# Performance work log

Measured on AMD Instinct MI355X. Metric: run time of the kernel, lower is better.

Reference implementation:

```python
import jax, jax.numpy as jnp
import numpy as np

N, H, I, B = 128, 128, 2, 8192

def _gru(x, h, Wih, Whh, bih, bhh):
    # torch.nn.GRUCell semantics; gates ordered (r, z, n)
    gi = x @ Wih.T + bih              # [B, 3H]
    gh = h @ Whh.T + bhh              # [B, 3H]
    ir, iz, ic = jnp.split(gi, 3, axis=1)
    hr, hz, hc = jnp.split(gh, 3, axis=1)
    r = jax.nn.sigmoid(ir + hr)
    z = jax.nn.sigmoid(iz + hz)
    n = jnp.tanh(ic + r * hc)
    return (1.0 - z) * n + z * h

def setup_inputs() -> dict:
    key = jax.random.key(0)
    ks = jax.random.split(key, 13)
    s = 0.1  # ~1/sqrt(H) init scale
    return {
        "inputs": jax.random.uniform(ks[0], (B, I), jnp.float32),
        "Wih0": jax.random.normal(ks[1], (N, 3 * H, I), jnp.float32) * s,
        "Whh0": jax.random.normal(ks[2], (N, 3 * H, H), jnp.float32) * s,
        "bih0": jax.random.normal(ks[3], (N, 3 * H), jnp.float32) * s,
        "bhh0": jax.random.normal(ks[4], (N, 3 * H), jnp.float32) * s,
        "Wih1": jax.random.normal(ks[5], (N, 3 * H, H), jnp.float32) * s,
        "Whh1": jax.random.normal(ks[6], (N, 3 * H, H), jnp.float32) * s,
        "bih1": jax.random.normal(ks[7], (N, 3 * H), jnp.float32) * s,
        "bhh1": jax.random.normal(ks[8], (N, 3 * H), jnp.float32) * s,
        "W1": jax.random.normal(ks[9], (N, H, H), jnp.float32) * s,
        "b1": jax.random.normal(ks[10], (N, H), jnp.float32) * s,
        "W2": jax.random.normal(ks[11], (N, I, H), jnp.float32) * s,
        "b2": jax.random.normal(ks[12], (N, I), jnp.float32) * s,
    }

def reference(inputs, Wih0, Whh0, bih0, bhh0, Wih1, Whh1, bih1, bhh1, W1, b1, W2, b2):
    batch = inputs.shape[0]
    h0 = jnp.zeros((batch, H), inputs.dtype)
    sample_keys = jax.random.split(jax.random.key(42), N)

    def step(carry, xs):
        inp, h1, h2 = carry
        (wih0, whh0, bi0, bh0, wih1, whh1, bi1, bh1, w1, bb1, w2, bb2, k) = xs
        h1 = _gru(inp, h1, wih0, whh0, bi0, bh0)
        h2 = _gru(h1, h2, wih1, whh1, bi1, bh1)
        s = jnp.cos(h2) + 1e-10
        hdn = jax.nn.relu(s @ w1.T + bb1)
        p = jax.nn.softmax(hdn @ w2.T + bb2, axis=1) + 1e-10  # probs + eps, as in torch
        sample = jax.lax.stop_gradient(jax.random.categorical(k, jnp.log(p)))
        nxt = jax.nn.one_hot(sample, I, dtype=p.dtype)
        return (nxt, h1, h2), p

    xs = (Wih0, Whh0, bih0, bhh0, Wih1, Whh1, bih1, bhh1, W1, b1, W2, b2, sample_keys)
    _, probs = jax.lax.scan(step, (inputs, h0, h0), xs)  # probs: [N, B, I]
    return jnp.transpose(probs, (1, 0, 2))  # [B, N, I]
```

## Files before the change

### kernel.cpp

```cpp
#include <hip/hip_runtime.h>
#include <cstdint>


namespace {

constexpr int NSTEPS = 128;
constexpr int HDIM = 128;
constexpr int G3H = 384;

constexpr int BTM = 32;
constexpr int THM = 512;
constexpr int S0P = 385;
constexpr int S1P = 513;

constexpr int BT = 16;
constexpr int THREADS = 256;
constexpr int HP = 132;
constexpr int SP = 516;

typedef _Float16 half8 __attribute__((ext_vector_type(8)));
typedef float f32x4 __attribute__((ext_vector_type(4)));

constexpr float LO_SCALE = 4096.0f;
constexpr float LO_INV = 2.44140625e-4f;
constexpr float F16_MIN_NORM = 6.104e-5f;
constexpr float LOG2E = 1.4426950408889634f;
constexpr float INV2PI = 0.15915494309189535f;

__device__ __forceinline__ void split_f16(float x, _Float16& a1, _Float16& a2s) {
  _Float16 h = (fabsf(x) < F16_MIN_NORM) ? (_Float16)0.0f : (_Float16)x;
  a1 = h;
  a2s = (_Float16)((x - (float)h) * LO_SCALE);
}

__device__ __forceinline__ void tf2x32(uint32_t k0, uint32_t k1,
                                       uint32_t x0, uint32_t x1,
                                       uint32_t& o0, uint32_t& o1) {
  const uint32_t ks2 = k0 ^ k1 ^ 0x1BD11BDAu;
  uint32_t v0 = x0 + k0;
  uint32_t v1 = x1 + k1;
  const uint32_t ks[3] = {k0, k1, ks2};
  const uint32_t rotA[4] = {13u, 15u, 26u, 6u};
  const uint32_t rotB[4] = {17u, 29u, 16u, 24u};
#pragma unroll
  for (int i = 0; i < 5; ++i) {
#pragma unroll
    for (int j = 0; j < 4; ++j) {
      const uint32_t r = (i & 1) ? rotB[j] : rotA[j];
      v0 += v1;
      v1 = (v1 << r) | (v1 >> (32u - r));
      v1 ^= v0;
    }
    v0 += ks[(i + 1) % 3];
    v1 += ks[(i + 2) % 3] + (uint32_t)(i + 1);
  }
  o0 = v0;
  o1 = v1;
}

__device__ __forceinline__ float u01_from_bits(uint32_t bits) {
  const float tiny = 1.1754943508222875e-38f;
  float f = __uint_as_float((bits >> 9) | 0x3F800000u) - 1.0f;
  float u = f * (1.0f - tiny) + tiny;
  return fmaxf(tiny, u);
}

__device__ __forceinline__ float fexp2(float x) { return __builtin_amdgcn_exp2f(x); }
__device__ __forceinline__ float frcp(float x) { return __builtin_amdgcn_rcpf(x); }
__device__ __forceinline__ float sigmoidf(float x) {
  return frcp(1.0f + fexp2(-LOG2E * x));
}
__device__ __forceinline__ float ftanhf(float x) {
  return 1.0f - 2.0f * frcp(1.0f + fexp2((2.0f * LOG2E) * x));
}
__device__ __forceinline__ float fcosx(float x) {
  return __builtin_amdgcn_cosf(x * INV2PI);
}

__device__ __forceinline__ float dot4(const float4 a, const float4 b, float c) {
  c = fmaf(a.x, b.x, c);
  c = fmaf(a.y, b.y, c);
  c = fmaf(a.z, b.z, c);
  c = fmaf(a.w, b.w, c);
  return c;
}

__device__ __forceinline__ void load_Afrag(const _Float16* arr, int lane,
                                           half8 (&A)[2][4]) {
#pragma unroll
  for (int mt = 0; mt < 2; ++mt)
#pragma unroll
    for (int kt = 0; kt < 4; ++kt)
      A[mt][kt] = *(const half8*)(arr + mt * 2048 + (kt * 64 + lane) * 8);
}

__device__ __forceinline__ void load_B(const _Float16* __restrict__ B1,
                                       const _Float16* __restrict__ B2,
                                       int jt, int lane,
                                       half8 (&b1)[4], half8 (&b2)[4]) {
#pragma unroll
  for (int kt = 0; kt < 4; ++kt) {
    const size_t o = ((size_t)(jt * 4 + kt) * 64 + lane) * 8;
    b1[kt] = *(const half8*)(B1 + o);
    b2[kt] = *(const half8*)(B2 + o);
  }
}

__device__ __forceinline__ void mfma_regs(const half8 (&A1)[2][4],
                                          const half8 (&A2)[2][4],
                                          const half8 (&b1)[4],
                                          const half8 (&b2)[4],
                                          f32x4 (&c1)[2], f32x4 (&c2)[2]) {
#pragma unroll
  for (int kt = 0; kt < 4; ++kt)
#pragma unroll
    for (int mt = 0; mt < 2; ++mt) {
      c1[mt] = __builtin_amdgcn_mfma_f32_16x16x32_f16(A1[mt][kt], b1[kt], c1[mt], 0, 0, 0);
      c2[mt] = __builtin_amdgcn_mfma_f32_16x16x32_f16(A1[mt][kt], b2[kt], c2[mt], 0, 0, 0);
      c2[mt] = __builtin_amdgcn_mfma_f32_16x16x32_f16(A2[mt][kt], b1[kt], c2[mt], 0, 0, 0);
    }
}

}

extern "C" __global__ __launch_bounds__(256)
void preprocess_split_kernel(const float* __restrict__ src,
                             _Float16* __restrict__ d1,
                             _Float16* __restrict__ d2,
                             int total, int JT) {
  const int idx = blockIdx.x * 256 + threadIdx.x;
  if (idx >= total) return;
  const int lane = idx & 63;
  const int kt = (idx >> 6) & 3;
  const int rest = idx >> 8;
  const int jt = rest % JT;
  const int nstep = rest / JT;

  const int j = jt * 16 + (lane & 15);
  const int k0 = kt * 32 + ((lane >> 4) << 3);
  const float* p = src + ((size_t)nstep * (JT * 16) + j) * 128 + k0;
  const float4 w0 = *(const float4*)p;
  const float4 w1 = *(const float4*)(p + 4);
  const float xs[8] = {w0.x, w0.y, w0.z, w0.w, w1.x, w1.y, w1.z, w1.w};

  half8 o1, o2;
#pragma unroll
  for (int t = 0; t < 8; ++t) {
    _Float16 a1, a2s;
    split_f16(xs[t], a1, a2s);
    o1[t] = a1;
    o2[t] = a2s;
  }
  *(half8*)(d1 + (size_t)idx * 8) = o1;
  *(half8*)(d2 + (size_t)idx * 8) = o2;
}

extern "C" __global__ __launch_bounds__(512, 2)
void rnn_wavefn_mfma_kernel(const float* __restrict__ inputs,
                            const float* __restrict__ Wih0,
                            const float* __restrict__ bih0,
                            const float* __restrict__ bhh0,
                            const float* __restrict__ bih1,
                            const float* __restrict__ bhh1,
                            const float* __restrict__ b1,
                            const float* __restrict__ W2,
                            const float* __restrict__ b2,
                            const _Float16* __restrict__ Whh0_1,
                            const _Float16* __restrict__ Whh0_2,
                            const _Float16* __restrict__ Wih1_1,
                            const _Float16* __restrict__ Wih1_2,
                            const _Float16* __restrict__ Whh1_1,
                            const _Float16* __restrict__ Whh1_2,
                            const _Float16* __restrict__ W1_1,
                            const _Float16* __restrict__ W1_2,
                            float* __restrict__ out) {
  __shared__ __align__(16) float S0[BTM][S0P];
  __shared__ float S1[BTM][S1P];
  __shared__ _Float16 h1A1[4096], h1A2[4096];
  __shared__ _Float16 h2A1[4096], h2A2[4096];
  __shared__ float xin[BTM][2];
  __shared__ uint32_t skey[NSTEPS][2];

  _Float16* const csA1 = (_Float16*)&S0[0][0];
  _Float16* const csA2 = csA1 + 4096;

  const int tid = threadIdx.x;
  const int b0 = blockIdx.x * BTM;
  const int wv = tid >> 6;
  const int lane = tid & 63;
  const int lm = lane & 15;
  const int m0 = (lane >> 4) * 4;

  const int cb = tid & 31;
  const int ct5 = tid >> 5;
  const int d0 = ct5 * 8;
  const int ibase = ((cb >> 4) * 2048 +
                     (((ct5 >> 2) << 6) + ((ct5 & 3) << 4) + (cb & 15)) * 8);

  float h1r[8], h2r[8];
#pragma unroll
  for (int i = 0; i < 8; ++i) { h1r[i] = 0.0f; h2r[i] = 0.0f; }
  for (int i = tid; i < 4096; i += THM) {
    h1A1[i] = (_Float16)0.0f; h1A2[i] = (_Float16)0.0f;
    h2A1[i] = (_Float16)0.0f; h2A2[i] = (_Float16)0.0f;
  }
  if (tid < BTM * 2) {
    xin[tid >> 1][tid & 1] = inputs[(b0 + (tid >> 1)) * 2 + (tid & 1)];
  }
  if (tid < NSTEPS) {
    uint32_t a, bk;
    tf2x32(0u, 42u, 0u, (uint32_t)tid, a, bk);
    skey[tid][0] = a;
    skey[tid][1] = bk;
  }
  __syncthreads();

  auto do_out = [&](int np) {
    const float* __restrict__ W2p = W2 + (size_t)np * 2 * HDIM;
    const float* __restrict__ b2p = b2 + (size_t)np * 2;
    const int ln = tid & 15;
    const int ob = tid >> 4;
    const int kb = ln * 8;
    float a0 = 0.0f, a1 = 0.0f;
#pragma unroll
    for (int k = 0; k < 8; ++k) {
      const float hd = S1[ob][384 + kb + k];
      a0 = fmaf(W2p[kb + k], hd, a0);
      a1 = fmaf(W2p[HDIM + kb + k], hd, a1);
    }
#pragma unroll
    for (int off = 8; off >= 1; off >>= 1) {
      a0 += __shfl_xor(a0, off, 16);
      a1 += __shfl_xor(a1, off, 16);
    }
    if (ln < 2) {
      const float l0 = a0 + b2p[0];
      const float l1 = a1 + b2p[1];
      const float m = fmaxf(l0, l1);
      const float e0 = expf(l0 - m);
      const float e1 = expf(l1 - m);
      const float sum = e0 + e1;
      const float p0 = e0 / sum + 1e-10f;
      const float p1 = e1 / sum + 1e-10f;
      const int gb = b0 + ob;
      uint32_t o0, o1;
      tf2x32(skey[np][0], skey[np][1], 0u, (uint32_t)(2 * gb + ln), o0, o1);
      const float u = u01_from_bits(o0 ^ o1);
      const float g = -logf(-logf(u));
      const float zv = logf((ln == 0) ? p0 : p1) + g;
      const float zo = __shfl_xor(zv, 1, 16);
      if (ln == 0) {
        out[((size_t)gb * NSTEPS + np) * 2 + 0] = p0;
        out[((size_t)gb * NSTEPS + np) * 2 + 1] = p1;
        const int smp = (zo > zv) ? 1 : 0;
        xin[ob][0] = (smp == 0) ? 1.0f : 0.0f;
        xin[ob][1] = (smp == 1) ? 1.0f : 0.0f;
      }
    }
  };

  half8 Bb1[2][4], Bb2[2][4];
  load_B(Whh0_1, Whh0_2, wv * 3, lane, Bb1[0], Bb2[0]);

  for (int n = 0; n < NSTEPS; ++n) {
    const float* __restrict__ Wih0n = Wih0 + (size_t)n * G3H * 2;
    const float* __restrict__ bih0n = bih0 + (size_t)n * G3H;
    const float* __restrict__ bhh0n = bhh0 + (size_t)n * G3H;
    const float* __restrict__ bih1n = bih1 + (size_t)n * G3H;
    const float* __restrict__ bhh1n = bhh1 + (size_t)n * G3H;
    const float* __restrict__ b1n = b1 + (size_t)n * HDIM;
    const size_t fo3 = (size_t)n * 49152;
    const size_t fo1 = (size_t)n * 16384;

    {
      half8 A1[2][4], A2[2][4];
      load_Afrag(h1A1, lane, A1);
      load_Afrag(h1A2, lane, A2);
      float bv[6];
#pragma unroll
      for (int t = 0; t < 6; ++t)
        bv[t] = ((t < 3) ? bhh0n : bhh1n)[(wv * 3 + (t % 3)) * 16 + lm];
#pragma unroll
      for (int t = 0; t < 6; ++t) {
        const int cur = t & 1;
        if (t < 5) {
          const int tn = t + 1;
          const _Float16* nB1 = (tn < 3) ? (Whh0_1 + fo3) : (Whh1_1 + fo3);
          const _Float16* nB2 = (tn < 3) ? (Whh0_2 + fo3) : (Whh1_2 + fo3);
          load_B(nB1, nB2, wv * 3 + (tn % 3), lane, Bb1[cur ^ 1], Bb2[cur ^ 1]);
        }
        if (t == 3) {
          load_Afrag(h2A1, lane, A1);
          load_Afrag(h2A2, lane, A2);
        }
        const int jt = wv * 3 + (t % 3);
        f32x4 c1[2] = {{0.f,0.f,0.f,0.f},{0.f,0.f,0.f,0.f}};
        f32x4 c2[2] = {{0.f,0.f,0.f,0.f},{0.f,0.f,0.f,0.f}};
        mfma_regs(A1, A2, Bb1[cur], Bb2[cur], c1, c2);
        const int col = jt * 16 + lm;
        if (t < 3) {
#pragma unroll
          for (int mt = 0; mt < 2; ++mt)
#pragma unroll
            for (int r = 0; r < 4; ++r)
              S0[mt * 16 + m0 + r][col] = bv[t] + fmaf(c2[mt][r], LO_INV, c1[mt][r]);
        } else {
#pragma unroll
          for (int mt = 0; mt < 2; ++mt)
#pragma unroll
            for (int r = 0; r < 4; ++r)
              S1[mt * 16 + m0 + r][col] = bv[t] + fmaf(c2[mt][r], LO_INV, c1[mt][r]);
        }
      }
    }
    if (n > 0) do_out(n - 1);
    __syncthreads();

    {
      load_B(Wih1_1 + fo3, Wih1_2 + fo3, wv * 3, lane, Bb1[0], Bb2[0]);
      const float x0 = xin[cb][0];
      const float x1 = xin[cb][1];
      float wr[16], wz[16], wn[16], br[8], bz[8], bn[8];
#pragma unroll
      for (int q = 0; q < 4; ++q) {
        *(float4*)&wr[q * 4] = *(const float4*)(Wih0n + d0 * 2 + q * 4);
        *(float4*)&wz[q * 4] = *(const float4*)(Wih0n + (d0 + 128) * 2 + q * 4);
        *(float4*)&wn[q * 4] = *(const float4*)(Wih0n + (d0 + 256) * 2 + q * 4);
      }
      *(float4*)&br[0] = *(const float4*)(bih0n + d0);
      *(float4*)&br[4] = *(const float4*)(bih0n + d0 + 4);
      *(float4*)&bz[0] = *(const float4*)(bih0n + 128 + d0);
      *(float4*)&bz[4] = *(const float4*)(bih0n + 128 + d0 + 4);
      *(float4*)&bn[0] = *(const float4*)(bih0n + 256 + d0);
      *(float4*)&bn[4] = *(const float4*)(bih0n + 256 + d0 + 4);
      half8 o1, o2;
#pragma unroll
      for (int j = 0; j < 8; ++j) {
        const int d = d0 + j;
        const float gir = fmaf(wr[2 * j], x0, fmaf(wr[2 * j + 1], x1, br[j]));
        const float giz = fmaf(wz[2 * j], x0, fmaf(wz[2 * j + 1], x1, bz[j]));
        const float gin = fmaf(wn[2 * j], x0, fmaf(wn[2 * j + 1], x1, bn[j]));
        const float r = sigmoidf(gir + S0[cb][d]);
        const float z = sigmoidf(giz + S0[cb][d + 128]);
        const float nn = ftanhf(gin + r * S0[cb][d + 256]);
        const float h1n = (1.0f - z) * nn + z * h1r[j];
        h1r[j] = h1n;
        _Float16 a1, a2s;
        split_f16(h1n, a1, a2s);
        o1[j] = a1;
        o2[j] = a2s;
      }
      *(half8*)(h1A1 + ibase) = o1;
      *(half8*)(h1A2 + ibase) = o2;
    }
    __syncthreads();

    {
      half8 A1[2][4], A2[2][4];
      load_Afrag(h1A1, lane, A1);
      load_Afrag(h1A2, lane, A2);
      float bv[3];
#pragma unroll
      for (int t = 0; t < 3; ++t) bv[t] = bih1n[(wv * 3 + t) * 16 + lm];
#pragma unroll
      for (int t = 0; t < 3; ++t) {
        const int cur = t & 1;
        if (t < 2)
          load_B(Wih1_1 + fo3, Wih1_2 + fo3, wv * 3 + t + 1, lane,
                 Bb1[cur ^ 1], Bb2[cur ^ 1]);
        const int jt = wv * 3 + t;
        f32x4 c1[2] = {{0.f,0.f,0.f,0.f},{0.f,0.f,0.f,0.f}};
        f32x4 c2[2] = {{0.f,0.f,0.f,0.f},{0.f,0.f,0.f,0.f}};
        mfma_regs(A1, A2, Bb1[cur], Bb2[cur], c1, c2);
        const int col = jt * 16 + lm;
        if (jt < 16) {
#pragma unroll
          for (int mt = 0; mt < 2; ++mt)
#pragma unroll
            for (int r = 0; r < 4; ++r)
              S1[mt * 16 + m0 + r][col] += bv[t] + fmaf(c2[mt][r], LO_INV, c1[mt][r]);
        } else {
#pragma unroll
          for (int mt = 0; mt < 2; ++mt)
#pragma unroll
            for (int r = 0; r < 4; ++r)
              S1[mt * 16 + m0 + r][col + 128] = bv[t] + fmaf(c2[mt][r], LO_INV, c1[mt][r]);
        }
      }
    }
    __syncthreads();

    half8 hb1[4], hb2[4];
    {
      load_B(W1_1 + fo1, W1_2 + fo1, wv, lane, hb1, hb2);
      const size_t fo3n = (size_t)((n + 1 < NSTEPS) ? n + 1 : n) * 49152;
      load_B(Whh0_1 + fo3n, Whh0_2 + fo3n, wv * 3, lane, Bb1[0], Bb2[0]);
      half8 o1, o2, p1, p2;
#pragma unroll
      for (int j = 0; j < 8; ++j) {
        const int d = d0 + j;
        const float r = sigmoidf(S1[cb][d]);
        const float z = sigmoidf(S1[cb][d + 128]);
        const float nn = ftanhf(S1[cb][d + 384] + r * S1[cb][d + 256]);
        const float h2n = (1.0f - z) * nn + z * h2r[j];
        h2r[j] = h2n;
        _Float16 a1, a2s;
        split_f16(h2n, a1, a2s);
        o1[j] = a1;
        o2[j] = a2s;
        const float cv = fcosx(h2n) + 1e-10f;
        split_f16(cv, a1, a2s);
        p1[j] = a1;
        p2[j] = a2s;
      }
      *(half8*)(h2A1 + ibase) = o1;
      *(half8*)(h2A2 + ibase) = o2;
      *(half8*)(csA1 + ibase) = p1;
      *(half8*)(csA2 + ibase) = p2;
    }
    __syncthreads();

    {
      const float bias = b1n[wv * 16 + lm];
      half8 A1[2][4], A2[2][4];
      load_Afrag(csA1, lane, A1);
      load_Afrag(csA2, lane, A2);
      f32x4 c1[2] = {{0.f,0.f,0.f,0.f},{0.f,0.f,0.f,0.f}};
      f32x4 c2[2] = {{0.f,0.f,0.f,0.f},{0.f,0.f,0.f,0.f}};
      mfma_regs(A1, A2, hb1, hb2, c1, c2);
      const int col = wv * 16 + lm;
#pragma unroll
      for (int mt = 0; mt < 2; ++mt)
#pragma unroll
        for (int r = 0; r < 4; ++r)
          S1[mt * 16 + m0 + r][384 + col] =
              fmaxf(bias + fmaf(c2[mt][r], LO_INV, c1[mt][r]), 0.0f);
    }
    __syncthreads();
  }

  do_out(NSTEPS - 1);
}

extern "C" __global__ __launch_bounds__(256, 2)
void rnn_wavefn_fp32_kernel(const float* __restrict__ inputs,
                            const float* __restrict__ Wih0,
                            const float* __restrict__ Whh0,
                            const float* __restrict__ bih0,
                            const float* __restrict__ bhh0,
                            const float* __restrict__ Wih1,
                            const float* __restrict__ Whh1,
                            const float* __restrict__ bih1,
                            const float* __restrict__ bhh1,
                            const float* __restrict__ W1,
                            const float* __restrict__ b1,
                            const float* __restrict__ W2,
                            const float* __restrict__ b2,
                            float* __restrict__ out) {
  __shared__ float h1[BT][HP];
  __shared__ float h2[BT][HP];
  __shared__ float S[BT][SP];
  __shared__ float xin[BT][2];

  const int tid = threadIdx.x;
  const int b0 = blockIdx.x * BT;
  const int tj = tid >> 2;
  const int tq = tid & 3;

  for (int i = tid; i < BT * HP; i += THREADS) {
    ((float*)h1)[i] = 0.0f;
    ((float*)h2)[i] = 0.0f;
  }
  if (tid < BT * 2) {
    xin[tid >> 1][tid & 1] = inputs[(b0 + (tid >> 1)) * 2 + (tid & 1)];
  }
  __syncthreads();

  for (int n = 0; n < NSTEPS; ++n) {
    const float* __restrict__ Wih0n = Wih0 + (size_t)n * G3H * 2;
    const float* __restrict__ Whh0n = Whh0 + (size_t)n * G3H * HDIM;
    const float* __restrict__ bih0n = bih0 + (size_t)n * G3H;
    const float* __restrict__ bhh0n = bhh0 + (size_t)n * G3H;
    const float* __restrict__ Wih1n = Wih1 + (size_t)n * G3H * HDIM;
    const float* __restrict__ Whh1n = Whh1 + (size_t)n * G3H * HDIM;
    const float* __restrict__ bih1n = bih1 + (size_t)n * G3H;
    const float* __restrict__ bhh1n = bhh1 + (size_t)n * G3H;
    const float* __restrict__ W1n = W1 + (size_t)n * HDIM * HDIM;
    const float* __restrict__ b1n = b1 + (size_t)n * HDIM;
    const float* __restrict__ W2n = W2 + (size_t)n * 2 * HDIM;
    const float* __restrict__ b2n = b2 + (size_t)n * 2;

    {
      float acc[6][4];
#pragma unroll
      for (int g = 0; g < 6; ++g) {
        const float bias = bhh0n[tj + g * 64];
#pragma unroll
        for (int i = 0; i < 4; ++i) acc[g][i] = bias;
      }
      for (int kk = 0; kk < HDIM; kk += 16) {
#pragma unroll
        for (int s = 0; s < 4; ++s) {
          const int k = kk + s * 4;
          float4 w[6];
#pragma unroll
          for (int g = 0; g < 6; ++g)
            w[g] = *(const float4*)(Whh0n + (size_t)(tj + g * 64) * HDIM + k);
#pragma unroll
          for (int i = 0; i < 4; ++i) {
            const float4 hv = *(const float4*)&h1[tq + 4 * i][k];
#pragma unroll
            for (int g = 0; g < 6; ++g) acc[g][i] = dot4(w[g], hv, acc[g][i]);
          }
        }
      }
#pragma unroll
      for (int g = 0; g < 6; ++g)
#pragma unroll
        for (int i = 0; i < 4; ++i) S[tq + 4 * i][tj + g * 64] = acc[g][i];
    }
    __syncthreads();

#pragma unroll
    for (int rep = 0; rep < (BT * HDIM) / THREADS; ++rep) {
      const int idx = tid + rep * THREADS;
      const int b = idx >> 7;
      const int d = idx & 127;
      const float x0 = xin[b][0];
      const float x1 = xin[b][1];
      const float gir = fmaf(Wih0n[d * 2 + 0], x0, fmaf(Wih0n[d * 2 + 1], x1, bih0n[d]));
      const float giz = fmaf(Wih0n[(d + 128) * 2 + 0], x0,
                             fmaf(Wih0n[(d + 128) * 2 + 1], x1, bih0n[d + 128]));
      const float gin = fmaf(Wih0n[(d + 256) * 2 + 0], x0,
                             fmaf(Wih0n[(d + 256) * 2 + 1], x1, bih0n[d + 256]));
      const float r = sigmoidf(gir + S[b][d]);
      const float z = sigmoidf(giz + S[b][d + 128]);
      const float nn = tanhf(gin + r * S[b][d + 256]);
      h1[b][d] = (1.0f - z) * nn + z * h1[b][d];
    }
    __syncthreads();

    {
      float acc[6][4];
#pragma unroll
      for (int g = 0; g < 6; ++g) {
        const float bias = bhh1n[tj + g * 64];
#pragma unroll
        for (int i = 0; i < 4; ++i) acc[g][i] = bias;
      }
      for (int kk = 0; kk < HDIM; kk += 16) {
#pragma unroll
        for (int s = 0; s < 4; ++s) {
          const int k = kk + s * 4;
          float4 w[6];
#pragma unroll
          for (int g = 0; g < 6; ++g)
            w[g] = *(const float4*)(Whh1n + (size_t)(tj + g * 64) * HDIM + k);
#pragma unroll
          for (int i = 0; i < 4; ++i) {
            const float4 hv = *(const float4*)&h2[tq + 4 * i][k];
#pragma unroll
            for (int g = 0; g < 6; ++g) acc[g][i] = dot4(w[g], hv, acc[g][i]);
          }
        }
      }
#pragma unroll
      for (int g = 0; g < 6; ++g)
#pragma unroll
        for (int i = 0; i < 4; ++i) S[tq + 4 * i][tj + g * 64] = acc[g][i];
    }

    {
      float acc[6][4];
#pragma unroll
      for (int g = 0; g < 6; ++g) {
        const float bias = bih1n[tj + g * 64];
#pragma unroll
        for (int i = 0; i < 4; ++i) acc[g][i] = bias;
      }
      for (int kk = 0; kk < HDIM; kk += 16) {
#pragma unroll
        for (int s = 0; s < 4; ++s) {
          const int k = kk + s * 4;
          float4 w[6];
#pragma unroll
          for (int g = 0; g < 6; ++g)
            w[g] = *(const float4*)(Wih1n + (size_t)(tj + g * 64) * HDIM + k);
#pragma unroll
          for (int i = 0; i < 4; ++i) {
            const float4 hv = *(const float4*)&h1[tq + 4 * i][k];
#pragma unroll
            for (int g = 0; g < 6; ++g) acc[g][i] = dot4(w[g], hv, acc[g][i]);
          }
        }
      }
#pragma unroll
      for (int g = 0; g < 6; ++g) {
        const int row = tj + g * 64;
#pragma unroll
        for (int i = 0; i < 4; ++i) {
          if (row < 256) S[tq + 4 * i][row] += acc[g][i];
          else           S[tq + 4 * i][row + 128] = acc[g][i];
        }
      }
    }
    __syncthreads();

#pragma unroll
    for (int rep = 0; rep < (BT * HDIM) / THREADS; ++rep) {
      const int idx = tid + rep * THREADS;
      const int b = idx >> 7;
      const int d = idx & 127;
      const float r = sigmoidf(S[b][d]);
      const float z = sigmoidf(S[b][d + 128]);
      const float nn = tanhf(S[b][d + 384] + r * S[b][d + 256]);
      const float h2n = (1.0f - z) * nn + z * h2[b][d];
      h2[b][d] = h2n;
      S[b][d] = cosf(h2n) + 1e-10f;
    }
    __syncthreads();

    {
      float acc[2][4];
#pragma unroll
      for (int g = 0; g < 2; ++g) {
        const float bias = b1n[tj + g * 64];
#pragma unroll
        for (int i = 0; i < 4; ++i) acc[g][i] = bias;
      }
      for (int kk = 0; kk < HDIM; kk += 16) {
#pragma unroll
        for (int s = 0; s < 4; ++s) {
          const int k = kk + s * 4;
          float4 w[2];
          w[0] = *(const float4*)(W1n + (size_t)(tj)*HDIM + k);
          w[1] = *(const float4*)(W1n + (size_t)(tj + 64) * HDIM + k);
#pragma unroll
          for (int i = 0; i < 4; ++i) {
            const float4 sv = *(const float4*)&S[tq + 4 * i][k];
            acc[0][i] = dot4(w[0], sv, acc[0][i]);
            acc[1][i] = dot4(w[1], sv, acc[1][i]);
          }
        }
      }
#pragma unroll
      for (int g = 0; g < 2; ++g)
#pragma unroll
        for (int i = 0; i < 4; ++i)
          S[tq + 4 * i][384 + tj + g * 64] = fmaxf(acc[g][i], 0.0f);
    }
    __syncthreads();

    {
      const int ln = tid & 15;
      const int b = tid >> 4;
      const int kb = ln * 8;
      float a0 = 0.0f, a1 = 0.0f;
#pragma unroll
      for (int k = 0; k < 8; ++k) {
        const float hd = S[b][384 + kb + k];
        a0 = fmaf(W2n[kb + k], hd, a0);
        a1 = fmaf(W2n[HDIM + kb + k], hd, a1);
      }
#pragma unroll
      for (int off = 8; off >= 1; off >>= 1) {
        a0 += __shfl_xor(a0, off, 16);
        a1 += __shfl_xor(a1, off, 16);
      }
      if (ln == 0) {
        const float l0 = a0 + b2n[0];
        const float l1 = a1 + b2n[1];
        const float m = fmaxf(l0, l1);
        const float e0 = expf(l0 - m);
        const float e1 = expf(l1 - m);
        const float sum = e0 + e1;
        const float p0 = e0 / sum + 1e-10f;
        const float p1 = e1 / sum + 1e-10f;
        const int gb = b0 + b;
        out[((size_t)gb * NSTEPS + n) * 2 + 0] = p0;
        out[((size_t)gb * NSTEPS + n) * 2 + 1] = p1;

        uint32_t k0n, k1n;
        tf2x32(0u, 42u, 0u, (uint32_t)n, k0n, k1n);
        uint32_t o0, o1;
        tf2x32(k0n, k1n, 0u, (uint32_t)(2 * gb), o0, o1);
        const float u0 = u01_from_bits(o0 ^ o1);
        tf2x32(k0n, k1n, 0u, (uint32_t)(2 * gb + 1), o0, o1);
        const float u1 = u01_from_bits(o0 ^ o1);
        const float g0 = -logf(-logf(u0));
        const float g1 = -logf(-logf(u1));
        const float z0 = logf(p0) + g0;
        const float z1 = logf(p1) + g1;
        const int smp = (z1 > z0) ? 1 : 0;
        xin[b][0] = (smp == 0) ? 1.0f : 0.0f;
        xin[b][1] = (smp == 1) ? 1.0f : 0.0f;
      }
    }
    __syncthreads();
  }
}

extern "C" void kernel_launch(void* const* d_in, const int* in_sizes, int n_in,
                              void* d_out, int out_size, void* d_ws, size_t ws_size,
                              hipStream_t stream) {
  (void)in_sizes; (void)n_in; (void)out_size;
  const float* inputs = (const float*)d_in[0];
  const float* Wih0 = (const float*)d_in[1];
  const float* Whh0 = (const float*)d_in[2];
  const float* bih0 = (const float*)d_in[3];
  const float* bhh0 = (const float*)d_in[4];
  const float* Wih1 = (const float*)d_in[5];
  const float* Whh1 = (const float*)d_in[6];
  const float* bih1 = (const float*)d_in[7];
  const float* bhh1 = (const float*)d_in[8];
  const float* W1 = (const float*)d_in[9];
  const float* b1 = (const float*)d_in[10];
  const float* W2 = (const float*)d_in[11];
  const float* b2 = (const float*)d_in[12];
  float* out = (float*)d_out;

  constexpr size_t EB = 6291456;
  constexpr size_t EW1 = 2097152;
  constexpr size_t WS_NEEDED = (6 * EB + 2 * EW1) * sizeof(_Float16);

  if (ws_size >= WS_NEEDED) {
    _Float16* w = (_Float16*)d_ws;
    _Float16* Whh0_1 = w;
    _Float16* Whh0_2 = w + EB;
    _Float16* Wih1_1 = w + 2 * EB;
    _Float16* Wih1_2 = w + 3 * EB;
    _Float16* Whh1_1 = w + 4 * EB;
    _Float16* Whh1_2 = w + 5 * EB;
    _Float16* W1_1 = w + 6 * EB;
    _Float16* W1_2 = w + 6 * EB + EW1;

    hipLaunchKernelGGL(preprocess_split_kernel, dim3(3072), dim3(256), 0, stream,
                       Whh0, Whh0_1, Whh0_2, 786432, 24);
    hipLaunchKernelGGL(preprocess_split_kernel, dim3(3072), dim3(256), 0, stream,
                       Wih1, Wih1_1, Wih1_2, 786432, 24);
    hipLaunchKernelGGL(preprocess_split_kernel, dim3(3072), dim3(256), 0, stream,
                       Whh1, Whh1_1, Whh1_2, 786432, 24);
    hipLaunchKernelGGL(preprocess_split_kernel, dim3(1024), dim3(256), 0, stream,
                       W1, W1_1, W1_2, 262144, 8);
    hipLaunchKernelGGL(rnn_wavefn_mfma_kernel, dim3(8192 / BTM), dim3(THM), 0, stream,
                       inputs, Wih0, bih0, bhh0, bih1, bhh1, b1, W2, b2,
                       Whh0_1, Whh0_2, Wih1_1, Wih1_2, Whh1_1, Whh1_2, W1_1, W1_2,
                       out);
  } else {
    hipLaunchKernelGGL(rnn_wavefn_fp32_kernel, dim3(8192 / BT), dim3(THREADS), 0, stream,
                       inputs, Wih0, Whh0, bih0, bhh0, Wih1, Whh1, bih1, bhh1,
                       W1, b1, W2, b2, out);
  }
}
```

Measured before the change: 1.577 ms.

## Double block to 1024 threads and split GRU gate tiles across 16 waves

```diff
diff --git a/kernel.cpp b/kernel.cpp
--- a/kernel.cpp
+++ b/kernel.cpp
@@ -9,7 +9,7 @@
 constexpr int G3H = 384;
 
 constexpr int BTM = 32;
-constexpr int THM = 512;
+constexpr int THM = 1024;
 constexpr int S0P = 385;
 constexpr int S1P = 513;
 
@@ -19,6 +19,7 @@
 constexpr int SP = 516;
 
 typedef _Float16 half8 __attribute__((ext_vector_type(8)));
+typedef _Float16 half4 __attribute__((ext_vector_type(4)));
 typedef float f32x4 __attribute__((ext_vector_type(4)));
 
 constexpr float LO_SCALE = 4096.0f;
@@ -155,7 +156,7 @@
   *(half8*)(d2 + (size_t)idx * 8) = o2;
 }
 
-extern "C" __global__ __launch_bounds__(512, 2)
+extern "C" __global__ __launch_bounds__(1024, 4)
 void rnn_wavefn_mfma_kernel(const float* __restrict__ inputs,
                             const float* __restrict__ Wih0,
                             const float* __restrict__ bih0,
@@ -193,13 +194,14 @@
 
   const int cb = tid & 31;
   const int ct5 = tid >> 5;
-  const int d0 = ct5 * 8;
-  const int ibase = ((cb >> 4) * 2048 +
-                     (((ct5 >> 2) << 6) + ((ct5 & 3) << 4) + (cb & 15)) * 8);
-
-  float h1r[8], h2r[8];
-#pragma unroll
-  for (int i = 0; i < 8; ++i) { h1r[i] = 0.0f; h2r[i] = 0.0f; }
+  const int d0 = ct5 * 4;
+  const int ibase4 = (cb >> 4) * 2048 +
+                     (((ct5 >> 3) << 6) + (((ct5 >> 1) & 3) << 4) + (cb & 15)) * 8 +
+                     (ct5 & 1) * 4;
+
+  float h1r[4], h2r[4];
+#pragma unroll
+  for (int i = 0; i < 4; ++i) { h1r[i] = 0.0f; h2r[i] = 0.0f; }
   for (int i = tid; i < 4096; i += THM) {
     h1A1[i] = (_Float16)0.0f; h1A2[i] = (_Float16)0.0f;
     h2A1[i] = (_Float16)0.0f; h2A2[i] = (_Float16)0.0f;
@@ -218,20 +220,20 @@
   auto do_out = [&](int np) {
     const float* __restrict__ W2p = W2 + (size_t)np * 2 * HDIM;
     const float* __restrict__ b2p = b2 + (size_t)np * 2;
-    const int ln = tid & 15;
-    const int ob = tid >> 4;
-    const int kb = ln * 8;
+    const int ln = tid & 31;
+    const int ob = tid >> 5;
+    const int kb = ln * 4;
     float a0 = 0.0f, a1 = 0.0f;
 #pragma unroll
-    for (int k = 0; k < 8; ++k) {
+    for (int k = 0; k < 4; ++k) {
       const float hd = S1[ob][384 + kb + k];
       a0 = fmaf(W2p[kb + k], hd, a0);
       a1 = fmaf(W2p[HDIM + kb + k], hd, a1);
     }
 #pragma unroll
-    for (int off = 8; off >= 1; off >>= 1) {
-      a0 += __shfl_xor(a0, off, 16);
-      a1 += __shfl_xor(a1, off, 16);
+    for (int off = 16; off >= 1; off >>= 1) {
+      a0 += __shfl_xor(a0, off, 32);
+      a1 += __shfl_xor(a1, off, 32);
     }
     if (ln < 2) {
       const float l0 = a0 + b2p[0];
@@ -248,7 +250,7 @@
       const float u = u01_from_bits(o0 ^ o1);
       const float g = -logf(-logf(u));
       const float zv = logf((ln == 0) ? p0 : p1) + g;
-      const float zo = __shfl_xor(zv, 1, 16);
+      const float zo = __shfl_xor(zv, 1, 32);
       if (ln == 0) {
         out[((size_t)gb * NSTEPS + np) * 2 + 0] = p0;
         out[((size_t)gb * NSTEPS + np) * 2 + 1] = p1;
@@ -260,7 +262,12 @@
   };
 
   half8 Bb1[2][4], Bb2[2][4];
-  load_B(Whh0_1, Whh0_2, wv * 3, lane, Bb1[0], Bb2[0]);
+  {
+    const int mj = (wv < 8) ? wv * 3 : (wv - 8) * 3;
+    const _Float16* p1 = (wv < 8) ? Whh0_1 : Whh1_1;
+    const _Float16* p2 = (wv < 8) ? Whh0_2 : Whh1_2;
+    load_B(p1, p2, mj, lane, Bb1[0], Bb2[0]);
+  }
 
   for (int n = 0; n < NSTEPS; ++n) {
     const float* __restrict__ Wih0n = Wih0 + (size_t)n * G3H * 2;
@@ -274,31 +281,30 @@
 
     {
       half8 A1[2][4], A2[2][4];
-      load_Afrag(h1A1, lane, A1);
-      load_Afrag(h1A2, lane, A2);
-      float bv[6];
-#pragma unroll
-      for (int t = 0; t < 6; ++t)
-        bv[t] = ((t < 3) ? bhh0n : bhh1n)[(wv * 3 + (t % 3)) * 16 + lm];
-#pragma unroll
-      for (int t = 0; t < 6; ++t) {
+      if (wv < 8) {
+        load_Afrag(h1A1, lane, A1);
+        load_Afrag(h1A2, lane, A2);
+      } else {
+        load_Afrag(h2A1, lane, A1);
+        load_Afrag(h2A2, lane, A2);
+      }
+      const int wj = (wv < 8) ? wv * 3 : (wv - 8) * 3;
+      const _Float16* p1 = ((wv < 8) ? Whh0_1 : Whh1_1) + fo3;
+      const _Float16* p2 = ((wv < 8) ? Whh0_2 : Whh1_2) + fo3;
+      const float* __restrict__ bb = (wv < 8) ? bhh0n : bhh1n;
+      float bv[3];
+#pragma unroll
+      for (int t = 0; t < 3; ++t) bv[t] = bb[(wj + t) * 16 + lm];
+#pragma unroll
+      for (int t = 0; t < 3; ++t) {
         const int cur = t & 1;
-        if (t < 5) {
-          const int tn = t + 1;
-          const _Float16* nB1 = (tn < 3) ? (Whh0_1 + fo3) : (Whh1_1 + fo3);
-          const _Float16* nB2 = (tn < 3) ? (Whh0_2 + fo3) : (Whh1_2 + fo3);
-          load_B(nB1, nB2, wv * 3 + (tn % 3), lane, Bb1[cur ^ 1], Bb2[cur ^ 1]);
-        }
-        if (t == 3) {
-          load_Afrag(h2A1, lane, A1);
-          load_Afrag(h2A2, lane, A2);
-        }
-        const int jt = wv * 3 + (t % 3);
+        if (t < 2)
+          load_B(p1, p2, wj + t + 1, lane, Bb1[cur ^ 1], Bb2[cur ^ 1]);
         f32x4 c1[2] = {{0.f,0.f,0.f,0.f},{0.f,0.f,0.f,0.f}};
         f32x4 c2[2] = {{0.f,0.f,0.f,0.f},{0.f,0.f,0.f,0.f}};
         mfma_regs(A1, A2, Bb1[cur], Bb2[cur], c1, c2);
-        const int col = jt * 16 + lm;
-        if (t < 3) {
+        const int col = (wj + t) * 16 + lm;
+        if (wv < 8) {
 #pragma unroll
           for (int mt = 0; mt < 2; ++mt)
 #pragma unroll
@@ -317,25 +323,23 @@
     __syncthreads();
 
     {
-      load_B(Wih1_1 + fo3, Wih1_2 + fo3, wv * 3, lane, Bb1[0], Bb2[0]);
+      const int gj0 = (wv < 8) ? (2 * wv) : (wv + 8);
+      load_B(Wih1_1 + fo3, Wih1_2 + fo3, gj0, lane, Bb1[0], Bb2[0]);
       const float x0 = xin[cb][0];
       const float x1 = xin[cb][1];
-      float wr[16], wz[16], wn[16], br[8], bz[8], bn[8];
-#pragma unroll
-      for (int q = 0; q < 4; ++q) {
+      float wr[8], wz[8], wn[8], br[4], bz[4], bn[4];
+#pragma unroll
+      for (int q = 0; q < 2; ++q) {
         *(float4*)&wr[q * 4] = *(const float4*)(Wih0n + d0 * 2 + q * 4);
         *(float4*)&wz[q * 4] = *(const float4*)(Wih0n + (d0 + 128) * 2 + q * 4);
         *(float4*)&wn[q * 4] = *(const float4*)(Wih0n + (d0 + 256) * 2 + q * 4);
       }
       *(float4*)&br[0] = *(const float4*)(bih0n + d0);
-      *(float4*)&br[4] = *(const float4*)(bih0n + d0 + 4);
       *(float4*)&bz[0] = *(const float4*)(bih0n + 128 + d0);
-      *(float4*)&bz[4] = *(const float4*)(bih0n + 128 + d0 + 4);
       *(float4*)&bn[0] = *(const float4*)(bih0n + 256 + d0);
-      *(float4*)&bn[4] = *(const float4*)(bih0n + 256 + d0 + 4);
-      half8 o1, o2;
-#pragma unroll
-      for (int j = 0; j < 8; ++j) {
+      half4 o1, o2;
+#pragma unroll
+      for (int j = 0; j < 4; ++j) {
         const int d = d0 + j;
         const float gir = fmaf(wr[2 * j], x0, fmaf(wr[2 * j + 1], x1, br[j]));
         const float giz = fmaf(wz[2 * j], x0, fmaf(wz[2 * j + 1], x1, bz[j]));
@@ -350,8 +354,8 @@
         o1[j] = a1;
         o2[j] = a2s;
       }
-      *(half8*)(h1A1 + ibase) = o1;
-      *(half8*)(h1A2 + ibase) = o2;
+      *(half4*)(h1A1 + ibase4) = o1;
+      *(half4*)(h1A2 + ibase4) = o2;
     }
     __syncthreads();
 
@@ -359,45 +363,51 @@
       half8 A1[2][4], A2[2][4];
       load_Afrag(h1A1, lane, A1);
       load_Afrag(h1A2, lane, A2);
-      float bv[3];
-#pragma unroll
-      for (int t = 0; t < 3; ++t) bv[t] = bih1n[(wv * 3 + t) * 16 + lm];
-#pragma unroll
-      for (int t = 0; t < 3; ++t) {
-        const int cur = t & 1;
-        if (t < 2)
-          load_B(Wih1_1 + fo3, Wih1_2 + fo3, wv * 3 + t + 1, lane,
-                 Bb1[cur ^ 1], Bb2[cur ^ 1]);
-        const int jt = wv * 3 + t;
+      if (wv < 8) {
+        float bv[2];
+        bv[0] = bih1n[(2 * wv) * 16 + lm];
+        bv[1] = bih1n[(2 * wv + 1) * 16 + lm];
+#pragma unroll
+        for (int t = 0; t < 2; ++t) {
+          if (t < 1)
+            load_B(Wih1_1 + fo3, Wih1_2 + fo3, 2 * wv + 1, lane, Bb1[1], Bb2[1]);
+          f32x4 c1[2] = {{0.f,0.f,0.f,0.f},{0.f,0.f,0.f,0.f}};
+          f32x4 c2[2] = {{0.f,0.f,0.f,0.f},{0.f,0.f,0.f,0.f}};
+          mfma_regs(A1, A2, Bb1[t], Bb2[t], c1, c2);
+          const int col = (2 * wv + t) * 16 + lm;
+#pragma unroll
+          for (int mt = 0; mt < 2; ++mt)
+#pragma unroll
+            for (int r = 0; r < 4; ++r)
+              S1[mt * 16 + m0 + r][col] += bv[t] + fmaf(c2[mt][r], LO_INV, c1[mt][r]);
+        }
+      } else {
+        const int jt = wv + 8;
+        const float bvn = bih1n[jt * 16 + lm];
         f32x4 c1[2] = {{0.f,0.f,0.f,0.f},{0.f,0.f,0.f,0.f}};
         f32x4 c2[2] = {{0.f,0.f,0.f,0.f},{0.f,0.f,0.f,0.f}};
-        mfma_regs(A1, A2, Bb1[cur], Bb2[cur], c1, c2);
+        mfma_regs(A1, A2, Bb1[0], Bb2[0], c1, c2);
         const int col = jt * 16 + lm;
-        if (jt < 16) {
-#pragma unroll
-          for (int mt = 0; mt < 2; ++mt)
-#pragma unroll
-            for (int r = 0; r < 4; ++r)
-              S1[mt * 16 + m0 + r][col] += bv[t] + fmaf(c2[mt][r], LO_INV, c1[mt][r]);
-        } else {
-#pragma unroll
-          for (int mt = 0; mt < 2; ++mt)
-#pragma unroll
-            for (int r = 0; r < 4; ++r)
-              S1[mt * 16 + m0 + r][col + 128] = bv[t] + fmaf(c2[mt][r], LO_INV, c1[mt][r]);
-        }
+#pragma unroll
+        for (int mt = 0; mt < 2; ++mt)
+#pragma unroll
+          for (int r = 0; r < 4; ++r)
+            S1[mt * 16 + m0 + r][col + 128] = bvn + fmaf(c2[mt][r], LO_INV, c1[mt][r]);
       }
     }
     __syncthreads();
 
     half8 hb1[4], hb2[4];
     {
-      load_B(W1_1 + fo1, W1_2 + fo1, wv, lane, hb1, hb2);
+      if (wv < 8) load_B(W1_1 + fo1, W1_2 + fo1, wv, lane, hb1, hb2);
       const size_t fo3n = (size_t)((n + 1 < NSTEPS) ? n + 1 : n) * 49152;
-      load_B(Whh0_1 + fo3n, Whh0_2 + fo3n, wv * 3, lane, Bb1[0], Bb2[0]);
-      half8 o1, o2, p1, p2;
-#pragma unroll
-      for (int j = 0; j < 8; ++j) {
+      const int mj = (wv < 8) ? wv * 3 : (wv - 8) * 3;
+      const _Float16* q1 = ((wv < 8) ? Whh0_1 : Whh1_1) + fo3n;
+      const _Float16* q2 = ((wv < 8) ? Whh0_2 : Whh1_2) + fo3n;
+      load_B(q1, q2, mj, lane, Bb1[0], Bb2[0]);
+      half4 o1, o2, p1, p2;
+#pragma unroll
+      for (int j = 0; j < 4; ++j) {
         const int d = d0 + j;
         const float r = sigmoidf(S1[cb][d]);
         const float z = sigmoidf(S1[cb][d + 128]);
@@ -413,14 +423,14 @@
         p1[j] = a1;
         p2[j] = a2s;
       }
-      *(half8*)(h2A1 + ibase) = o1;
-      *(half8*)(h2A2 + ibase) = o2;
-      *(half8*)(csA1 + ibase) = p1;
-      *(half8*)(csA2 + ibase) = p2;
-    }
-    __syncthreads();
-
-    {
+      *(half4*)(h2A1 + ibase4) = o1;
+      *(half4*)(h2A2 + ibase4) = o2;
+      *(half4*)(csA1 + ibase4) = p1;
+      *(half4*)(csA2 + ibase4) = p2;
+    }
+    __syncthreads();
+
+    if (wv < 8) {
       const float bias = b1n[wv * 16 + lm];
       half8 A1[2][4], A2[2][4];
       load_Afrag(csA1, lane, A1);
```

After: 3.641 ms. 2.31x slower.

## Widen block to 12 waves and repartition MFMA gate tiles across waves

Applied to the files above, without the earlier changes.

```diff
diff --git a/kernel.cpp b/kernel.cpp
--- a/kernel.cpp
+++ b/kernel.cpp
@@ -9,7 +9,7 @@
 constexpr int G3H = 384;
 
 constexpr int BTM = 32;
-constexpr int THM = 512;
+constexpr int THM = 768;
 constexpr int S0P = 385;
 constexpr int S1P = 513;
 
@@ -155,7 +155,7 @@
   *(half8*)(d2 + (size_t)idx * 8) = o2;
 }
 
-extern "C" __global__ __launch_bounds__(512, 2)
+extern "C" __global__ __launch_bounds__(768, 1)
 void rnn_wavefn_mfma_kernel(const float* __restrict__ inputs,
                             const float* __restrict__ Wih0,
                             const float* __restrict__ bih0,
@@ -192,7 +192,7 @@
   const int m0 = (lane >> 4) * 4;
 
   const int cb = tid & 31;
-  const int ct5 = tid >> 5;
+  const int ct5 = (tid >> 5) & 15;
   const int d0 = ct5 * 8;
   const int ibase = ((cb >> 4) * 2048 +
                      (((ct5 >> 2) << 6) + ((ct5 & 3) << 4) + (cb & 15)) * 8);
@@ -220,47 +220,54 @@
     const float* __restrict__ b2p = b2 + (size_t)np * 2;
     const int ln = tid & 15;
     const int ob = tid >> 4;
-    const int kb = ln * 8;
-    float a0 = 0.0f, a1 = 0.0f;
-#pragma unroll
-    for (int k = 0; k < 8; ++k) {
-      const float hd = S1[ob][384 + kb + k];
-      a0 = fmaf(W2p[kb + k], hd, a0);
-      a1 = fmaf(W2p[HDIM + kb + k], hd, a1);
-    }
-#pragma unroll
-    for (int off = 8; off >= 1; off >>= 1) {
-      a0 += __shfl_xor(a0, off, 16);
-      a1 += __shfl_xor(a1, off, 16);
-    }
-    if (ln < 2) {
-      const float l0 = a0 + b2p[0];
-      const float l1 = a1 + b2p[1];
-      const float m = fmaxf(l0, l1);
-      const float e0 = expf(l0 - m);
-      const float e1 = expf(l1 - m);
-      const float sum = e0 + e1;
-      const float p0 = e0 / sum + 1e-10f;
-      const float p1 = e1 / sum + 1e-10f;
-      const int gb = b0 + ob;
-      uint32_t o0, o1;
-      tf2x32(skey[np][0], skey[np][1], 0u, (uint32_t)(2 * gb + ln), o0, o1);
-      const float u = u01_from_bits(o0 ^ o1);
-      const float g = -logf(-logf(u));
-      const float zv = logf((ln == 0) ? p0 : p1) + g;
-      const float zo = __shfl_xor(zv, 1, 16);
-      if (ln == 0) {
-        out[((size_t)gb * NSTEPS + np) * 2 + 0] = p0;
-        out[((size_t)gb * NSTEPS + np) * 2 + 1] = p1;
-        const int smp = (zo > zv) ? 1 : 0;
-        xin[ob][0] = (smp == 0) ? 1.0f : 0.0f;
-        xin[ob][1] = (smp == 1) ? 1.0f : 0.0f;
+    if (ob < 32) {
+      const int kb = ln * 8;
+      float a0 = 0.0f, a1 = 0.0f;
+#pragma unroll
+      for (int k = 0; k < 8; ++k) {
+        const float hd = S1[ob][384 + kb + k];
+        a0 = fmaf(W2p[kb + k], hd, a0);
+        a1 = fmaf(W2p[HDIM + kb + k], hd, a1);
+      }
+#pragma unroll
+      for (int off = 8; off >= 1; off >>= 1) {
+        a0 += __shfl_xor(a0, off, 16);
+        a1 += __shfl_xor(a1, off, 16);
+      }
+      if (ln < 2) {
+        const float l0 = a0 + b2p[0];
+        const float l1 = a1 + b2p[1];
+        const float m = fmaxf(l0, l1);
+        const float e0 = expf(l0 - m);
+        const float e1 = expf(l1 - m);
+        const float sum = e0 + e1;
+        const float p0 = e0 / sum + 1e-10f;
+        const float p1 = e1 / sum + 1e-10f;
+        const int gb = b0 + ob;
+        uint32_t o0, o1;
+        tf2x32(skey[np][0], skey[np][1], 0u, (uint32_t)(2 * gb + ln), o0, o1);
+        const float u = u01_from_bits(o0 ^ o1);
+        const float g = -logf(-logf(u));
+        const float zv = logf((ln == 0) ? p0 : p1) + g;
+        const float zo = __shfl_xor(zv, 1, 16);
+        if (ln == 0) {
+          out[((size_t)gb * NSTEPS + np) * 2 + 0] = p0;
+          out[((size_t)gb * NSTEPS + np) * 2 + 1] = p1;
+          const int smp = (zo > zv) ? 1 : 0;
+          xin[ob][0] = (smp == 0) ? 1.0f : 0.0f;
+          xin[ob][1] = (smp == 1) ? 1.0f : 0.0f;
+        }
       }
     }
   };
 
   half8 Bb1[2][4], Bb2[2][4];
-  load_B(Whh0_1, Whh0_2, wv * 3, lane, Bb1[0], Bb2[0]);
+  {
+    const int mj = (wv < 6) ? wv * 4 : (wv - 6) * 4;
+    const _Float16* p1 = (wv < 6) ? Whh0_1 : Whh1_1;
+    const _Float16* p2 = (wv < 6) ? Whh0_2 : Whh1_2;
+    load_B(p1, p2, mj, lane, Bb1[0], Bb2[0]);
+  }
 
   for (int n = 0; n < NSTEPS; ++n) {
     const float* __restrict__ Wih0n = Wih0 + (size_t)n * G3H * 2;
@@ -274,31 +281,30 @@
 
     {
       half8 A1[2][4], A2[2][4];
-      load_Afrag(h1A1, lane, A1);
-      load_Afrag(h1A2, lane, A2);
-      float bv[6];
-#pragma unroll
-      for (int t = 0; t < 6; ++t)
-        bv[t] = ((t < 3) ? bhh0n : bhh1n)[(wv * 3 + (t % 3)) * 16 + lm];
-#pragma unroll
-      for (int t = 0; t < 6; ++t) {
+      if (wv < 6) {
+        load_Afrag(h1A1, lane, A1);
+        load_Afrag(h1A2, lane, A2);
+      } else {
+        load_Afrag(h2A1, lane, A1);
+        load_Afrag(h2A2, lane, A2);
+      }
+      const int wj = (wv < 6) ? wv * 4 : (wv - 6) * 4;
+      const _Float16* p1 = ((wv < 6) ? Whh0_1 : Whh1_1) + fo3;
+      const _Float16* p2 = ((wv < 6) ? Whh0_2 : Whh1_2) + fo3;
+      const float* __restrict__ bb = (wv < 6) ? bhh0n : bhh1n;
+      float bv[4];
+#pragma unroll
+      for (int t = 0; t < 4; ++t) bv[t] = bb[(wj + t) * 16 + lm];
+#pragma unroll
+      for (int t = 0; t < 4; ++t) {
         const int cur = t & 1;
-        if (t < 5) {
-          const int tn = t + 1;
-          const _Float16* nB1 = (tn < 3) ? (Whh0_1 + fo3) : (Whh1_1 + fo3);
-          const _Float16* nB2 = (tn < 3) ? (Whh0_2 + fo3) : (Whh1_2 + fo3);
-          load_B(nB1, nB2, wv * 3 + (tn % 3), lane, Bb1[cur ^ 1], Bb2[cur ^ 1]);
-        }
-        if (t == 3) {
-          load_Afrag(h2A1, lane, A1);
-          load_Afrag(h2A2, lane, A2);
-        }
-        const int jt = wv * 3 + (t % 3);
+        if (t < 3)
+          load_B(p1, p2, wj + t + 1, lane, Bb1[cur ^ 1], Bb2[cur ^ 1]);
         f32x4 c1[2] = {{0.f,0.f,0.f,0.f},{0.f,0.f,0.f,0.f}};
         f32x4 c2[2] = {{0.f,0.f,0.f,0.f},{0.f,0.f,0.f,0.f}};
         mfma_regs(A1, A2, Bb1[cur], Bb2[cur], c1, c2);
-        const int col = jt * 16 + lm;
-        if (t < 3) {
+        const int col = (wj + t) * 16 + lm;
+        if (wv < 6) {
 #pragma unroll
           for (int mt = 0; mt < 2; ++mt)
 #pragma unroll
@@ -317,41 +323,43 @@
     __syncthreads();
 
     {
-      load_B(Wih1_1 + fo3, Wih1_2 + fo3, wv * 3, lane, Bb1[0], Bb2[0]);
-      const float x0 = xin[cb][0];
-      const float x1 = xin[cb][1];
-      float wr[16], wz[16], wn[16], br[8], bz[8], bn[8];
-#pragma unroll
-      for (int q = 0; q < 4; ++q) {
-        *(float4*)&wr[q * 4] = *(const float4*)(Wih0n + d0 * 2 + q * 4);
-        *(float4*)&wz[q * 4] = *(const float4*)(Wih0n + (d0 + 128) * 2 + q * 4);
-        *(float4*)&wn[q * 4] = *(const float4*)(Wih0n + (d0 + 256) * 2 + q * 4);
-      }
-      *(float4*)&br[0] = *(const float4*)(bih0n + d0);
-      *(float4*)&br[4] = *(const float4*)(bih0n + d0 + 4);
-      *(float4*)&bz[0] = *(const float4*)(bih0n + 128 + d0);
-      *(float4*)&bz[4] = *(const float4*)(bih0n + 128 + d0 + 4);
-      *(float4*)&bn[0] = *(const float4*)(bih0n + 256 + d0);
-      *(float4*)&bn[4] = *(const float4*)(bih0n + 256 + d0 + 4);
-      half8 o1, o2;
-#pragma unroll
-      for (int j = 0; j < 8; ++j) {
-        const int d = d0 + j;
-        const float gir = fmaf(wr[2 * j], x0, fmaf(wr[2 * j + 1], x1, br[j]));
-        const float giz = fmaf(wz[2 * j], x0, fmaf(wz[2 * j + 1], x1, bz[j]));
-        const float gin = fmaf(wn[2 * j], x0, fmaf(wn[2 * j + 1], x1, bn[j]));
-        const float r = sigmoidf(gir + S0[cb][d]);
-        const float z = sigmoidf(giz + S0[cb][d + 128]);
-        const float nn = ftanhf(gin + r * S0[cb][d + 256]);
-        const float h1n = (1.0f - z) * nn + z * h1r[j];
-        h1r[j] = h1n;
-        _Float16 a1, a2s;
-        split_f16(h1n, a1, a2s);
-        o1[j] = a1;
-        o2[j] = a2s;
-      }
-      *(half8*)(h1A1 + ibase) = o1;
-      *(half8*)(h1A2 + ibase) = o2;
+      load_B(Wih1_1 + fo3, Wih1_2 + fo3, 2 * wv, lane, Bb1[0], Bb2[0]);
+      if (tid < 512) {
+        const float x0 = xin[cb][0];
+        const float x1 = xin[cb][1];
+        float wr[16], wz[16], wn[16], br[8], bz[8], bn[8];
+#pragma unroll
+        for (int q = 0; q < 4; ++q) {
+          *(float4*)&wr[q * 4] = *(const float4*)(Wih0n + d0 * 2 + q * 4);
+          *(float4*)&wz[q * 4] = *(const float4*)(Wih0n + (d0 + 128) * 2 + q * 4);
+          *(float4*)&wn[q * 4] = *(const float4*)(Wih0n + (d0 + 256) * 2 + q * 4);
+        }
+        *(float4*)&br[0] = *(const float4*)(bih0n + d0);
+        *(float4*)&br[4] = *(const float4*)(bih0n + d0 + 4);
+        *(float4*)&bz[0] = *(const float4*)(bih0n + 128 + d0);
+        *(float4*)&bz[4] = *(const float4*)(bih0n + 128 + d0 + 4);
+        *(float4*)&bn[0] = *(const float4*)(bih0n + 256 + d0);
+        *(float4*)&bn[4] = *(const float4*)(bih0n + 256 + d0 + 4);
+        half8 o1, o2;
+#pragma unroll
+        for (int j = 0; j < 8; ++j) {
+          const int d = d0 + j;
+          const float gir = fmaf(wr[2 * j], x0, fmaf(wr[2 * j + 1], x1, br[j]));
+          const float giz = fmaf(wz[2 * j], x0, fmaf(wz[2 * j + 1], x1, bz[j]));
+          const float gin = fmaf(wn[2 * j], x0, fmaf(wn[2 * j + 1], x1, bn[j]));
+          const float r = sigmoidf(gir + S0[cb][d]);
+          const float z = sigmoidf(giz + S0[cb][d + 128]);
+          const float nn = ftanhf(gin + r * S0[cb][d + 256]);
+          const float h1n = (1.0f - z) * nn + z * h1r[j];
+          h1r[j] = h1n;
+          _Float16 a1, a2s;
+          split_f16(h1n, a1, a2s);
+          o1[j] = a1;
+          o2[j] = a2s;
+        }
+        *(half8*)(h1A1 + ibase) = o1;
+        *(half8*)(h1A2 + ibase) = o2;
+      }
     }
     __syncthreads();
 
@@ -359,19 +367,17 @@
       half8 A1[2][4], A2[2][4];
       load_Afrag(h1A1, lane, A1);
       load_Afrag(h1A2, lane, A2);
-      float bv[3];
-#pragma unroll
-      for (int t = 0; t < 3; ++t) bv[t] = bih1n[(wv * 3 + t) * 16 + lm];
-#pragma unroll
-      for (int t = 0; t < 3; ++t) {
-        const int cur = t & 1;
-        if (t < 2)
-          load_B(Wih1_1 + fo3, Wih1_2 + fo3, wv * 3 + t + 1, lane,
-                 Bb1[cur ^ 1], Bb2[cur ^ 1]);
-        const int jt = wv * 3 + t;
+      float bv[2];
+      bv[0] = bih1n[(2 * wv) * 16 + lm];
+      bv[1] = bih1n[(2 * wv + 1) * 16 + lm];
+#pragma unroll
+      for (int t = 0; t < 2; ++t) {
+        if (t < 1)
+          load_B(Wih1_1 + fo3, Wih1_2 + fo3, 2 * wv + 1, lane, Bb1[1], Bb2[1]);
         f32x4 c1[2] = {{0.f,0.f,0.f,0.f},{0.f,0.f,0.f,0.f}};
         f32x4 c2[2] = {{0.f,0.f,0.f,0.f},{0.f,0.f,0.f,0.f}};
-        mfma_regs(A1, A2, Bb1[cur], Bb2[cur], c1, c2);
+        mfma_regs(A1, A2, Bb1[t], Bb2[t], c1, c2);
+        const int jt = 2 * wv + t;
         const int col = jt * 16 + lm;
         if (jt < 16) {
 #pragma unroll
@@ -392,35 +398,40 @@
 
     half8 hb1[4], hb2[4];
     {
-      load_B(W1_1 + fo1, W1_2 + fo1, wv, lane, hb1, hb2);
+      if (wv < 8) load_B(W1_1 + fo1, W1_2 + fo1, wv, lane, hb1, hb2);
       const size_t fo3n = (size_t)((n + 1 < NSTEPS) ? n + 1 : n) * 49152;
-      load_B(Whh0_1 + fo3n, Whh0_2 + fo3n, wv * 3, lane, Bb1[0], Bb2[0]);
-      half8 o1, o2, p1, p2;
-#pragma unroll
-      for (int j = 0; j < 8; ++j) {
-        const int d = d0 + j;
-        const float r = sigmoidf(S1[cb][d]);
-        const float z = sigmoidf(S1[cb][d + 128]);
-        const float nn = ftanhf(S1[cb][d + 384] + r * S1[cb][d + 256]);
-        const float h2n = (1.0f - z) * nn + z * h2r[j];
-        h2r[j] = h2n;
-        _Float16 a1, a2s;
-        split_f16(h2n, a1, a2s);
-        o1[j] = a1;
-        o2[j] = a2s;
-        const float cv = fcosx(h2n) + 1e-10f;
-        split_f16(cv, a1, a2s);
-        p1[j] = a1;
-        p2[j] = a2s;
-      }
-      *(half8*)(h2A1 + ibase) = o1;
-      *(half8*)(h2A2 + ibase) = o2;
-      *(half8*)(csA1 + ibase) = p1;
-      *(half8*)(csA2 + ibase) = p2;
-    }
-    __syncthreads();
-
-    {
+      const int mj = (wv < 6) ? wv * 4 : (wv - 6) * 4;
+      const _Float16* q1 = ((wv < 6) ? Whh0_1 : Whh1_1) + fo3n;
+      const _Float16* q2 = ((wv < 6) ? Whh0_2 : Whh1_2) + fo3n;
+      load_B(q1, q2, mj, lane, Bb1[0], Bb2[0]);
+      if (tid < 512) {
+        half8 o1, o2, p1, p2;
+#pragma unroll
+        for (int j = 0; j < 8; ++j) {
+          const int d = d0 + j;
+          const float r = sigmoidf(S1[cb][d]);
+          const float z = sigmoidf(S1[cb][d + 128]);
+          const float nn = ftanhf(S1[cb][d + 384] + r * S1[cb][d + 256]);
+          const float h2n = (1.0f - z) * nn + z * h2r[j];
+          h2r[j] = h2n;
+          _Float16 a1, a2s;
+          split_f16(h2n, a1, a2s);
+          o1[j] = a1;
+          o2[j] = a2s;
+          const float cv = fcosx(h2n) + 1e-10f;
+          split_f16(cv, a1, a2s);
+          p1[j] = a1;
+          p2[j] = a2s;
+        }
+        *(half8*)(h2A1 + ibase) = o1;
+        *(half8*)(h2A2 + ibase) = o2;
+        *(half8*)(csA1 + ibase) = p1;
+        *(half8*)(csA2 + ibase) = p2;
+      }
+    }
+    __syncthreads();
+
+    if (wv < 8) {
       const float bias = b1n[wv * 16 + lm];
       half8 A1[2][4], A2[2][4];
       load_Afrag(csA1, lane, A1);
```

New measurement: 3.151 ms. +99.7%, slower.
